# Kernel optimization log

Hardware: AMD Instinct MI355X
Metric: run time of the kernel (lower is better)

## Reference

```python
import jax, jax.numpy as jnp
import numpy as np

B, H, W, C = 128, 8, 32, 512
RNN = 512; EMB = 512; ATT = 512
VOCAB = 110          # vocab_size -> classes = VOCAB + 1
MAXLEN = 30          # loop runs MAXLEN + 1 steps


def setup_inputs() -> dict:
    key = jax.random.key(0)
    ks = jax.random.split(key, 16)
    w = lambda i, shape: jax.random.normal(ks[i], shape, jnp.float32) * 0.02
    return {
        "features": jax.random.normal(ks[0], (B, H, W, C), jnp.float32),
        "holistic": jax.random.normal(ks[1], (B, RNN), jnp.float32),
        "gt": jax.random.randint(ks[2], (B, MAXLEN + 1), 0, VOCAB + 1),
        "embed_W": w(3, (VOCAB + 1, EMB)),
        "k0": w(4, (EMB, 4 * RNN)), "rk0": w(5, (RNN, 4 * RNN)), "b0": jnp.zeros((4 * RNN,), jnp.float32),
        "k1": w(6, (RNN, 4 * RNN)), "rk1": w(7, (RNN, 4 * RNN)), "b1": jnp.zeros((4 * RNN,), jnp.float32),
        "Wh": w(8, (RNN, ATT)),                       # 1x1 conv on (B,1,1,RNN) == dense
        "Wf": w(9, (3, 3, C, ATT)), "bf": jnp.zeros((ATT,), jnp.float32),
        "wa": w(10, (ATT, 1)),                        # 1x1 conv -> scalar attention logit
        "out_W": w(11, (2 * RNN, VOCAB + 1)), "out_b": jnp.zeros((VOCAB + 1,), jnp.float32),
    }


def _lstm(x, h, c, k, rk, b):
    # Keras LSTMCell: gates order i, f, g(cell), o
    z = x @ k + h @ rk + b
    i, f, g, o = jnp.split(z, 4, axis=-1)
    c2 = jax.nn.sigmoid(f) * c + jax.nn.sigmoid(i) * jnp.tanh(g)
    h2 = jax.nn.sigmoid(o) * jnp.tanh(c2)
    return h2, c2


def reference(features, holistic, gt, embed_W, k0, rk0, b0, k1, rk1, b1,
              Wh, Wf, bf, wa, out_W, out_b):
    Bb, Hh, Ww, Cc = features.shape
    # features_projector (3x3 conv, SAME) is timestep-invariant: precompute once
    fproj = jax.lax.conv_general_dilated(
        features, Wf, (1, 1), "SAME",
        dimension_numbers=("NHWC", "HWIO", "NHWC")) + bf          # (B,H,W,ATT)

    zeros = jnp.zeros((Bb, RNN), features.dtype)
    # prime stacked LSTM with holistic vector (zero initial state)
    h0, c0 = _lstm(holistic, zeros, zeros, k0, rk0, b0)
    h1, c1 = _lstm(h0, zeros, zeros, k1, rk1, b1)

    # teacher forcing: step 0 uses SOS token = vocab_size+1 (out-of-range -> zero one-hot),
    # step t>0 uses gt[:, t-1]
    sos = jnp.full((1, Bb), VOCAB + 1, gt.dtype)
    symbols = jnp.concatenate([sos, gt[:, :MAXLEN].T], axis=0)     # (T, B), T = MAXLEN+1

    def step(carry, sym):
        h0, c0, h1, c1 = carry
        x = jax.nn.one_hot(sym, VOCAB + 1, dtype=features.dtype) @ embed_W   # (B, EMB)
        h0, c0 = _lstm(x, h0, c0, k0, rk0, b0)
        h1, c1 = _lstm(h0, h1, c1, k1, rk1, b1)
        # attention over conv feature map
        hp = h1 @ Wh                                               # (B, ATT)
        proj = jnp.tanh(fproj + hp[:, None, None, :])              # (B,H,W,ATT)
        att = (proj @ wa).reshape(Bb, Hh * Ww)                     # (B, H*W)
        att = jax.nn.softmax(att, axis=-1).reshape(Bb, Hh, Ww, 1)
        glimpse = jnp.sum(features * att, axis=(1, 2))             # (B, C)
        logits = jnp.concatenate([h1, glimpse], axis=-1) @ out_W + out_b
        return (h0, c0, h1, c1), logits

    _, logits = jax.lax.scan(step, (h0, c0, h1, c1), symbols)      # (T, B, VOCAB+1)
    return jnp.transpose(logits, (1, 0, 2))                        # (B, T, VOCAB+1)
```

## Files before the change

kernel.cpp:

```cpp
#include <hip/hip_runtime.h>


typedef __bf16 bf16;
typedef bf16 bf16x8 __attribute__((ext_vector_type(8)));
typedef float f32x4 __attribute__((ext_vector_type(4)));

#define MFMA16(a, b, c) __builtin_amdgcn_mfma_f32_16x16x32_bf16((a), (b), (c), 0, 0, 0)

__device__ __forceinline__ float b2f(unsigned short u) {
    return __uint_as_float(((unsigned int)u) << 16);
}
__device__ __forceinline__ unsigned short f2b(float f) {
    unsigned int x = __float_as_uint(f);
    unsigned int r = (x + 0x7fffu + ((x >> 16) & 1u)) >> 16;
    return (unsigned short)r;
}
__device__ __forceinline__ float exp2_raw(float x) {
    float r;
    asm("v_exp_f32 %0, %1" : "=v"(r) : "v"(x));
    return r;
}
__device__ __forceinline__ float tanh_fast(float x) {
    const float e = exp2_raw(2.885390082f * x);
    return 1.0f - 2.0f * __builtin_amdgcn_rcpf(e + 1.0f);
}
__device__ __forceinline__ float sig_fast(float x) {
    return __builtin_amdgcn_rcpf(1.0f + exp2_raw(-1.44269504f * x));
}
__device__ __forceinline__ void gl16(const ushort* g, ushort* l) {
    __builtin_amdgcn_global_load_lds(
        (const __attribute__((address_space(1))) void*)g,
        (__attribute__((address_space(3))) void*)l, 16, 0, 0);
}

__global__ void detect_dtype(const void* __restrict__ feat, int* __restrict__ flag) {
    if (threadIdx.x == 0 && blockIdx.x == 0) {
        const ushort* u = (const ushort*)feat;
        int cnt = 0;
        for (int i = 0; i < 128; i += 2) {
            const int e = (u[i] >> 7) & 0xFF;
            if (e >= 96 && e <= 150) ++cnt;
        }
        *flag = (cnt >= 40) ? 0 : 1;
    }
}

__global__ __launch_bounds__(256) void cvt_bf16(
    const void* __restrict__ src, ushort* __restrict__ dst, int n,
    const int* __restrict__ flag) {
    const int i = blockIdx.x * 256 + threadIdx.x;
    if (i >= n) return;
    if (*flag) dst[i] = f2b(((const float*)src)[i]);
    else       dst[i] = ((const ushort*)src)[i];
}

__global__ __launch_bounds__(256) void cvt_f32(
    const void* __restrict__ src, float* __restrict__ dst, int n,
    const int* __restrict__ flag) {
    const int i = blockIdx.x * 256 + threadIdx.x;
    if (i >= n) return;
    if (*flag) dst[i] = ((const float*)src)[i];
    else       dst[i] = b2f(((const ushort*)src)[i]);
}

__global__ __launch_bounds__(256) void build_featpad(
    const void* __restrict__ feat, ushort* __restrict__ featPad,
    const int* __restrict__ flag) {
    const int i = blockIdx.x * 256 + threadIdx.x;
    if (i >= 128 * 10 * 34 * 512) return;
    const int c = i & 511;
    const int xy = i >> 9;
    const int x = xy % 34;
    const int t2 = xy / 34;
    const int y = t2 % 10;
    const int b = t2 / 10;
    ushort v = 0;
    if (y >= 1 && y <= 8 && x >= 1 && x <= 32) {
        const size_t si = ((size_t)((b * 8 + y - 1) * 32 + (x - 1)) << 9) + c;
        v = *flag ? f2b(((const float*)feat)[si]) : ((const ushort*)feat)[si];
    }
    featPad[i] = v;
}

__global__ __launch_bounds__(256) void transpose_any(
    const void* __restrict__ in, ushort* __restrict__ out, int R, int C,
    const int* __restrict__ flag) {
    __shared__ float s[32][33];
    const int f32 = *flag;
    const int nbc = C >> 5;
    const int rb = blockIdx.x / nbc, cb = blockIdx.x % nbc;
    const int tx = threadIdx.x & 31, ty = threadIdx.x >> 5;
#pragma unroll
    for (int k = 0; k < 4; ++k) {
        const size_t idx = (size_t)(rb * 32 + ty + k * 8) * C + cb * 32 + tx;
        s[ty + k * 8][tx] = f32 ? ((const float*)in)[idx] : b2f(((const ushort*)in)[idx]);
    }
    __syncthreads();
#pragma unroll
    for (int k = 0; k < 4; ++k)
        out[(size_t)(cb * 32 + ty + k * 8) * R + rb * 32 + tx] = f2b(s[tx][ty + k * 8]);
}

__global__ __launch_bounds__(256) void woT_build(
    const float* __restrict__ outWf, ushort* __restrict__ WoTpad) {
    const int i = blockIdx.x * 256 + threadIdx.x;
    if (i >= 131072) return;
    const int v = i >> 10, k = i & 1023;
    WoTpad[i] = (v < 111) ? f2b(outWf[k * 111 + v]) : (ushort)0;
}

__global__ __launch_bounds__(256) void conv_fproj(
    const ushort* __restrict__ featPad, const ushort* __restrict__ WfT,
    const float* __restrict__ bff, ushort* __restrict__ fproj) {
    __shared__ __align__(16) ushort As[128 * 64];
    __shared__ __align__(16) ushort Bs[128 * 64];
    const int tid = threadIdx.x;
    const int nb = blockIdx.x >> 8;
    const int rb = blockIdx.x & 255;
    const int b = rb >> 1, p0 = (rb & 1) << 7;
    const int w = tid >> 6, lane = tid & 63, l15 = lane & 15, q = lane >> 4;
    const int wr = (w >> 1) << 6, wc = (w & 1) << 6;
    const int chunkoff = (((lane & 7) ^ (lane >> 3)) << 3);
    int aoff[4], boff[4];
#pragma unroll
    for (int i = 0; i < 4; ++i) {
        const int r = w * 32 + (lane >> 3) + i * 8;
        const int p = p0 + r;
        const int yy = p >> 5, xx = p & 31;
        aoff[i] = (((b * 10 + yy) * 34 + xx) << 9) + chunkoff;
        boff[i] = (nb * 128 + r) * 4608 + chunkoff;
    }
    const int swa = l15 & 7;
    f32x4 acc[4][4] = {};
    for (int kb = 0; kb < 72; ++kb) {
        const int tap = kb >> 3;
        const int dy = tap / 3, dx = tap - dy * 3;
        const int koffA = ((dy * 34 + dx) << 9) + ((kb & 7) << 6);
        const int koffB = kb * 64;
        __syncthreads();
#pragma unroll
        for (int i = 0; i < 4; ++i) {
            gl16(featPad + aoff[i] + koffA, &As[(w * 32 + i * 8) * 64]);
            gl16(WfT + boff[i] + koffB, &Bs[(w * 32 + i * 8) * 64]);
        }
        __syncthreads();
#pragma unroll
        for (int ks = 0; ks < 64; ks += 32) {
            const int cq = (ks >> 3) + q;
            const int col = ((cq ^ swa) << 3);
            bf16x8 af[4], bfr[4];
#pragma unroll
            for (int i = 0; i < 4; ++i) af[i] = *(const bf16x8*)&As[(wr + i * 16 + l15) * 64 + col];
#pragma unroll
            for (int j = 0; j < 4; ++j) bfr[j] = *(const bf16x8*)&Bs[(wc + j * 16 + l15) * 64 + col];
#pragma unroll
            for (int i = 0; i < 4; ++i)
#pragma unroll
                for (int j = 0; j < 4; ++j)
                    acc[i][j] = MFMA16(af[i], bfr[j], acc[i][j]);
        }
    }
    const int rowbase = rb * 128 + wr, colbase = nb * 128 + wc;
#pragma unroll
    for (int i = 0; i < 4; ++i)
#pragma unroll
        for (int j = 0; j < 4; ++j)
#pragma unroll
            for (int rr = 0; rr < 4; ++rr) {
                const int row = rowbase + i * 16 + q * 4 + rr;
                const int col = colbase + j * 16 + l15;
                fproj[(size_t)row * 512 + col] = f2b(acc[i][j][rr] + bff[col]);
            }
}

__global__ __launch_bounds__(256) void gemm_bt(
    const ushort* __restrict__ A, const ushort* __restrict__ BT,
    float* __restrict__ C, int M, int N, int K, int lda) {
    __shared__ __align__(16) bf16 As[128][72];
    __shared__ __align__(16) bf16 Bs[128][72];
    const int tid = threadIdx.x;
    const int nnb = N >> 7;
    const int rb = blockIdx.x / nnb, nb = blockIdx.x % nnb;
    const int ar = tid >> 1, ah = (tid & 1) << 5;
    const int w = tid >> 6, lane = tid & 63, l15 = lane & 15, q = lane >> 4;
    const int wr = (w >> 1) << 6, wc = (w & 1) << 6;
    const int r_glob = rb * 128 + ar;
    const bool aval = (r_glob < M);
    const int r_ld = aval ? r_glob : 0;
    f32x4 acc[4][4] = {};
    const int nkb = K >> 6;
    for (int kb = 0; kb < nkb; ++kb) {
        const uint4 z4 = {0u, 0u, 0u, 0u};
        const uint4* asrc = (const uint4*)(A + (size_t)r_ld * lda + kb * 64 + ah);
        uint4 a0 = asrc[0], a1 = asrc[1], a2 = asrc[2], a3 = asrc[3];
        if (!aval) { a0 = z4; a1 = z4; a2 = z4; a3 = z4; }
        const uint4* bsrc = (const uint4*)(BT + (size_t)(nb * 128 + ar) * K + kb * 64 + ah);
        uint4 b0v = bsrc[0], b1v = bsrc[1], b2v = bsrc[2], b3v = bsrc[3];
        __syncthreads();
        *(uint4*)&As[ar][ah] = a0;
        *(uint4*)&As[ar][ah + 8] = a1;
        *(uint4*)&As[ar][ah + 16] = a2;
        *(uint4*)&As[ar][ah + 24] = a3;
        *(uint4*)&Bs[ar][ah] = b0v;
        *(uint4*)&Bs[ar][ah + 8] = b1v;
        *(uint4*)&Bs[ar][ah + 16] = b2v;
        *(uint4*)&Bs[ar][ah + 24] = b3v;
        __syncthreads();
#pragma unroll
        for (int ks = 0; ks < 64; ks += 32) {
            bf16x8 af[4], bfr[4];
#pragma unroll
            for (int i = 0; i < 4; ++i) af[i] = *(const bf16x8*)&As[wr + i * 16 + l15][ks + q * 8];
#pragma unroll
            for (int j = 0; j < 4; ++j) bfr[j] = *(const bf16x8*)&Bs[wc + j * 16 + l15][ks + q * 8];
#pragma unroll
            for (int i = 0; i < 4; ++i)
#pragma unroll
                for (int j = 0; j < 4; ++j)
                    acc[i][j] = MFMA16(af[i], bfr[j], acc[i][j]);
        }
    }
#pragma unroll
    for (int i = 0; i < 4; ++i)
#pragma unroll
        for (int j = 0; j < 4; ++j)
#pragma unroll
            for (int rr = 0; rr < 4; ++rr) {
                const int row = rb * 128 + wr + i * 16 + q * 4 + rr;
                const int col = nb * 128 + wc + j * 16 + l15;
                if (row < M) C[(size_t)row * N + col] = acc[i][j][rr];
            }
}

__global__ __launch_bounds__(256) void lstm_stage(
    int t,
    const ushort* __restrict__ holistic, const int* __restrict__ gt,
    const float* __restrict__ b0f, const float* __restrict__ b1f,
    const ushort* __restrict__ k0T, const ushort* __restrict__ rk0T,
    const ushort* __restrict__ k1T, const ushort* __restrict__ rk1T,
    const float* __restrict__ E0,
    ushort* h0b0, ushort* h0b1, ushort* h1b0, ushort* h1b1,
    float* c0buf, float* c1buf, ushort* HG) {
    const int part = blockIdx.x >> 7;
    const int bi = blockIdx.x & 127;
    const ushort *A1 = nullptr, *A2 = nullptr, *B1 = nullptr, *B2 = nullptr;
    const float* bias = nullptr;
    ushort *hout = nullptr, *hout2 = nullptr;
    float* cbuf = nullptr;
    bool useC = false, useE = false;
    if (part == 0) {
        if (!(t == -2 || (t >= 0 && t <= 30))) return;
        bias = b0f; cbuf = c0buf;
        if (t == -2) { A1 = holistic; B1 = k0T; hout = h0b1; }
        else {
            A1 = ((t + 1) & 1) ? h0b1 : h0b0;
            B1 = rk0T;
            hout = (t & 1) ? h0b1 : h0b0;
            useC = true; useE = true;
        }
    } else {
        if (!(t == -1 || (t >= 1 && t <= 31))) return;
        bias = b1f; cbuf = c1buf;
        if (t == -1) { A1 = h0b1; B1 = k1T; hout = h1b1; }
        else {
            const int s = t - 1;
            A1 = (s & 1) ? h0b1 : h0b0;
            A2 = ((s + 1) & 1) ? h1b1 : h1b0;
            B1 = k1T; B2 = rk1T;
            hout = (s & 1) ? h1b1 : h1b0;
            hout2 = HG + (size_t)s * 131072;
            useC = true;
        }
    }
    const int m0 = (bi >> 5) << 5;
    const int cc0 = (bi & 31) << 4;
    const int tid = threadIdx.x;
    const int w = tid >> 6, lane = tid & 63, l15 = lane & 15, q = lane >> 4;
    __shared__ __align__(16) ushort As1[32 * 520];
    __shared__ __align__(16) ushort As2[32 * 520];
    __shared__ float zs[4][32][17];
#pragma unroll
    for (int it = 0; it < 8; ++it) {
        const int idx = tid + it * 256;
        const int row = idx >> 6, chv = idx & 63;
        *(uint4*)&As1[row * 520 + chv * 8] =
            *(const uint4*)(A1 + (size_t)(m0 + row) * 512 + chv * 8);
    }
    if (A2) {
#pragma unroll
        for (int it = 0; it < 8; ++it) {
            const int idx = tid + it * 256;
            const int row = idx >> 6, chv = idx & 63;
            *(uint4*)&As2[row * 520 + chv * 8] =
                *(const uint4*)(A2 + (size_t)(m0 + row) * 512 + chv * 8);
        }
    }
    __syncthreads();
    const int nkb = A2 ? 16 : 8;
    const size_t brow = (size_t)(w * 512 + cc0 + l15) * 512 + q * 8;
    auto bp = [&](int kb) -> const ushort* {
        const ushort* base = (kb < 8) ? B1 : B2;
        return base + brow + (kb & 7) * 64;
    };
    bf16x8 b0a = *(const bf16x8*)bp(0), b1a = *(const bf16x8*)(bp(0) + 32);
    bf16x8 b0b = *(const bf16x8*)bp(1), b1b = *(const bf16x8*)(bp(1) + 32);
    bf16x8 b0c = *(const bf16x8*)bp(2), b1c = *(const bf16x8*)(bp(2) + 32);
    f32x4 acc0 = {}, acc1 = {};
    for (int kb = 0; kb < nkb; ++kb) {
        const bf16x8 p0 = b0a, p1 = b1a;
        b0a = b0b; b1a = b1b; b0b = b0c; b1b = b1c;
        if (kb + 3 < nkb) {
            b0c = *(const bf16x8*)bp(kb + 3);
            b1c = *(const bf16x8*)(bp(kb + 3) + 32);
        }
        const ushort* asrc = (kb < 8) ? As1 : As2;
        const int kk = (kb & 7) * 64 + q * 8;
        bf16x8 a00 = *(const bf16x8*)&asrc[l15 * 520 + kk];
        bf16x8 a10 = *(const bf16x8*)&asrc[(16 + l15) * 520 + kk];
        bf16x8 a01 = *(const bf16x8*)&asrc[l15 * 520 + kk + 32];
        bf16x8 a11 = *(const bf16x8*)&asrc[(16 + l15) * 520 + kk + 32];
        acc0 = MFMA16(a00, p0, acc0);
        acc1 = MFMA16(a10, p0, acc1);
        acc0 = MFMA16(a01, p1, acc0);
        acc1 = MFMA16(a11, p1, acc1);
    }
#pragma unroll
    for (int rr = 0; rr < 4; ++rr) {
        zs[w][q * 4 + rr][l15] = acc0[rr];
        zs[w][16 + q * 4 + rr][l15] = acc1[rr];
    }
    __syncthreads();
#pragma unroll
    for (int it = 0; it < 2; ++it) {
        const int e = tid + it * 256;
        const int mm = e >> 4, cc = e & 15;
        const int brow2 = m0 + mm, col = cc0 + cc;
        float zi = zs[0][mm][cc] + bias[col];
        float zf = zs[1][mm][cc] + bias[512 + col];
        float zg = zs[2][mm][cc] + bias[1024 + col];
        float zo = zs[3][mm][cc] + bias[1536 + col];
        if (useE) {
            const int s = (t == 0) ? 111 : gt[brow2 * 31 + t - 1];
            if (s >= 0 && s < 111) {
                const float* er = E0 + (size_t)s * 2048;
                zi += er[col]; zf += er[512 + col]; zg += er[1024 + col]; zo += er[1536 + col];
            }
        }
        const float cp = useC ? cbuf[brow2 * 512 + col] : 0.0f;
        const float c2 = sig_fast(zf) * cp + sig_fast(zi) * tanh_fast(zg);
        const float h = sig_fast(zo) * tanh_fast(c2);
        cbuf[brow2 * 512 + col] = c2;
        hout[brow2 * 512 + col] = f2b(h);
        if (hout2) hout2[brow2 * 1024 + col] = f2b(h);
    }
}

__global__ __launch_bounds__(256) void att_logits(
    const ushort* __restrict__ fproj, const float* __restrict__ HP,
    const float* __restrict__ waf, float* __restrict__ attL) {
    __shared__ float hpS[16][512];
    __shared__ float waS[512];
    __shared__ float accS[128][17];
    const int tid = threadIdx.x;
    const int b = blockIdx.x >> 2, ph = (blockIdx.x >> 1) & 1, th = blockIdx.x & 1;
    const int t0 = th << 4, tc = th ? 15 : 16;
    const int pl = tid & 127, ch = tid >> 7;
    const int p = ph * 128 + pl;
    for (int i = tid; i < 16 * 512; i += 256) {
        const int tt = i >> 9, c = i & 511;
        hpS[tt][c] = (tt < tc) ? 2.885390082f * HP[((size_t)(t0 + tt) * 128 + b) * 512 + c] : 0.0f;
    }
    waS[tid] = -2.0f * waf[tid];
    if (tid < 256) waS[256 + tid] = -2.0f * waf[256 + tid];
    __syncthreads();
    float sumW = 0.f;
    {
        const float* wh = &waS[ch * 256];
        for (int c4 = 0; c4 < 64; ++c4) {
            const float4 wv = *(const float4*)&wh[c4 * 4];
            sumW += wv.x + wv.y + wv.z + wv.w;
        }
        sumW *= -0.5f;
    }
    float acc[16];
#pragma unroll
    for (int tt = 0; tt < 16; ++tt) acc[tt] = 0.f;
    const ushort* frow = fproj + (size_t)(b * 256 + p) * 512 + ch * 256;
    for (int c8 = 0; c8 < 32; ++c8) {
        const int cc = ch * 256 + c8 * 8;
        const uint4 fv = *(const uint4*)(frow + c8 * 8);
        float f[8];
        f[0] = b2f((unsigned short)(fv.x & 0xffff)); f[1] = b2f((unsigned short)(fv.x >> 16));
        f[2] = b2f((unsigned short)(fv.y & 0xffff)); f[3] = b2f((unsigned short)(fv.y >> 16));
        f[4] = b2f((unsigned short)(fv.z & 0xffff)); f[5] = b2f((unsigned short)(fv.z >> 16));
        f[6] = b2f((unsigned short)(fv.w & 0xffff)); f[7] = b2f((unsigned short)(fv.w >> 16));
#pragma unroll
        for (int j = 0; j < 8; ++j) f[j] *= 2.885390082f;
        const float4 w0 = *(const float4*)&waS[cc];
        const float4 w1 = *(const float4*)&waS[cc + 4];
#pragma unroll
        for (int tt = 0; tt < 16; ++tt) {
            const float4 h0 = *(const float4*)&hpS[tt][cc];
            const float4 h1 = *(const float4*)&hpS[tt][cc + 4];
            float s = acc[tt];
            s = fmaf(__builtin_amdgcn_rcpf(exp2_raw(f[0] + h0.x) + 1.0f), w0.x, s);
            s = fmaf(__builtin_amdgcn_rcpf(exp2_raw(f[1] + h0.y) + 1.0f), w0.y, s);
            s = fmaf(__builtin_amdgcn_rcpf(exp2_raw(f[2] + h0.z) + 1.0f), w0.z, s);
            s = fmaf(__builtin_amdgcn_rcpf(exp2_raw(f[3] + h0.w) + 1.0f), w0.w, s);
            s = fmaf(__builtin_amdgcn_rcpf(exp2_raw(f[4] + h1.x) + 1.0f), w1.x, s);
            s = fmaf(__builtin_amdgcn_rcpf(exp2_raw(f[5] + h1.y) + 1.0f), w1.y, s);
            s = fmaf(__builtin_amdgcn_rcpf(exp2_raw(f[6] + h1.z) + 1.0f), w1.z, s);
            s = fmaf(__builtin_amdgcn_rcpf(exp2_raw(f[7] + h1.w) + 1.0f), w1.w, s);
            acc[tt] = s;
        }
    }
    if (ch == 1) {
#pragma unroll
        for (int tt = 0; tt < 16; ++tt) accS[pl][tt] = acc[tt] + sumW;
    }
    __syncthreads();
    if (ch == 0) {
        for (int tt = 0; tt < tc; ++tt)
            attL[((size_t)(t0 + tt) * 128 + b) * 256 + p] = acc[tt] + sumW + accS[pl][tt];
    }
}

__global__ __launch_bounds__(256) void glimpse_kernel(
    const ushort* __restrict__ featPad, const float* __restrict__ attL,
    ushort* __restrict__ HG) {
    __shared__ __align__(16) float attT[256 * 36];
    const int tid = threadIdx.x;
    const int b = blockIdx.x >> 1, chh = blockIdx.x & 1;
    const int c0 = chh << 8;
    const int w = tid >> 6, lane = tid & 63;
    for (int i = tid; i < 31 * 256; i += 256) {
        const int tt = i >> 8, p = i & 255;
        attT[p * 36 + tt] = attL[((size_t)tt * 128 + b) * 256 + p];
    }
    __syncthreads();
    for (int tt = w; tt < 31; tt += 4) {
        float v0 = attT[lane * 36 + tt], v1 = attT[(lane + 64) * 36 + tt];
        float v2 = attT[(lane + 128) * 36 + tt], v3 = attT[(lane + 192) * 36 + tt];
        float mx = fmaxf(fmaxf(v0, v1), fmaxf(v2, v3));
#pragma unroll
        for (int m = 1; m < 64; m <<= 1) mx = fmaxf(mx, __shfl_xor(mx, m));
        const float e0 = exp2_raw((v0 - mx) * 1.44269504f);
        const float e1 = exp2_raw((v1 - mx) * 1.44269504f);
        const float e2 = exp2_raw((v2 - mx) * 1.44269504f);
        const float e3 = exp2_raw((v3 - mx) * 1.44269504f);
        float s = e0 + e1 + e2 + e3;
#pragma unroll
        for (int m = 1; m < 64; m <<= 1) s += __shfl_xor(s, m);
        const float r = 1.0f / s;
        attT[lane * 36 + tt] = e0 * r;  attT[(lane + 64) * 36 + tt] = e1 * r;
        attT[(lane + 128) * 36 + tt] = e2 * r;  attT[(lane + 192) * 36 + tt] = e3 * r;
    }
    __syncthreads();
    float acc[31];
#pragma unroll
    for (int tt = 0; tt < 31; ++tt) acc[tt] = 0.f;
    for (int p = 0; p < 256; ++p) {
        const size_t fi = (((size_t)(b * 10 + (p >> 5) + 1) * 34 + (p & 31) + 1) << 9) + c0 + tid;
        const float fv = b2f(featPad[fi]);
        const float4 a0 = *(const float4*)&attT[p * 36];
        const float4 a1 = *(const float4*)&attT[p * 36 + 4];
        const float4 a2 = *(const float4*)&attT[p * 36 + 8];
        const float4 a3 = *(const float4*)&attT[p * 36 + 12];
        const float4 a4 = *(const float4*)&attT[p * 36 + 16];
        const float4 a5 = *(const float4*)&attT[p * 36 + 20];
        const float4 a6 = *(const float4*)&attT[p * 36 + 24];
        const float4 a7 = *(const float4*)&attT[p * 36 + 28];
        acc[0] = fmaf(fv, a0.x, acc[0]);   acc[1] = fmaf(fv, a0.y, acc[1]);
        acc[2] = fmaf(fv, a0.z, acc[2]);   acc[3] = fmaf(fv, a0.w, acc[3]);
        acc[4] = fmaf(fv, a1.x, acc[4]);   acc[5] = fmaf(fv, a1.y, acc[5]);
        acc[6] = fmaf(fv, a1.z, acc[6]);   acc[7] = fmaf(fv, a1.w, acc[7]);
        acc[8] = fmaf(fv, a2.x, acc[8]);   acc[9] = fmaf(fv, a2.y, acc[9]);
        acc[10] = fmaf(fv, a2.z, acc[10]); acc[11] = fmaf(fv, a2.w, acc[11]);
        acc[12] = fmaf(fv, a3.x, acc[12]); acc[13] = fmaf(fv, a3.y, acc[13]);
        acc[14] = fmaf(fv, a3.z, acc[14]); acc[15] = fmaf(fv, a3.w, acc[15]);
        acc[16] = fmaf(fv, a4.x, acc[16]); acc[17] = fmaf(fv, a4.y, acc[17]);
        acc[18] = fmaf(fv, a4.z, acc[18]); acc[19] = fmaf(fv, a4.w, acc[19]);
        acc[20] = fmaf(fv, a5.x, acc[20]); acc[21] = fmaf(fv, a5.y, acc[21]);
        acc[22] = fmaf(fv, a5.z, acc[22]); acc[23] = fmaf(fv, a5.w, acc[23]);
        acc[24] = fmaf(fv, a6.x, acc[24]); acc[25] = fmaf(fv, a6.y, acc[25]);
        acc[26] = fmaf(fv, a6.z, acc[26]); acc[27] = fmaf(fv, a6.w, acc[27]);
        acc[28] = fmaf(fv, a7.x, acc[28]); acc[29] = fmaf(fv, a7.y, acc[29]);
        acc[30] = fmaf(fv, a7.z, acc[30]);
    }
#pragma unroll
    for (int tt = 0; tt < 31; ++tt)
        HG[((size_t)tt * 128 + b) * 1024 + 512 + c0 + tid] = f2b(acc[tt]);
}

__global__ __launch_bounds__(256) void logits_store(
    const float* __restrict__ C, const float* __restrict__ outBf,
    void* __restrict__ out, const int* __restrict__ flag) {
    const int i = blockIdx.x * 256 + threadIdx.x;
    if (i >= 3968 * 111) return;
    const int r = i / 111, v = i - r * 111;
    const int tt = r >> 7, b = r & 127;
    const float a = C[(size_t)r * 128 + v] + outBf[v];
    const size_t oi = ((size_t)b * 31 + tt) * 111 + v;
    if (*flag) ((float*)out)[oi] = a;
    else       ((ushort*)out)[oi] = f2b(a);
}

extern "C" void kernel_launch(void* const* d_in, const int* in_sizes, int n_in,
                              void* d_out, int out_size, void* d_ws, size_t ws_size,
                              hipStream_t stream) {
    (void)in_sizes; (void)n_in; (void)out_size;
    const void* features = d_in[0];
    const void* holistic = d_in[1];
    const int*  gt       = (const int*)d_in[2];
    const void* embed_W  = d_in[3];
    const void* k0 = d_in[4];
    const void* rk0 = d_in[5];
    const void* b0 = d_in[6];
    const void* k1 = d_in[7];
    const void* rk1 = d_in[8];
    const void* b1 = d_in[9];
    const void* Wh = d_in[10];
    const void* Wf = d_in[11];
    const void* bfv = d_in[12];
    const void* wa = d_in[13];
    const void* outW = d_in[14];
    const void* outB = d_in[15];

    char* ws = (char*)d_ws;
    size_t off = 0;
    auto take = [&](size_t bytes) -> char* {
        char* p = ws + off;
        off += (bytes + 255) & ~(size_t)255;
        return p;
    };
    int*    flag    = (int*)take(256);
    ushort* featPad = (ushort*)take(128ull * 10 * 34 * 512 * 2);
    ushort* holB  = (ushort*)take(65536ull * 2);
    ushort* embB  = (ushort*)take(56832ull * 2);
    float*  b0f   = (float*)take(2048ull * 4);
    float*  b1f   = (float*)take(2048ull * 4);
    float*  bff   = (float*)take(512ull * 4);
    float*  waf   = (float*)take(512ull * 4);
    float*  outBf = (float*)take(111ull * 4);
    float*  outWf = (float*)take(113664ull * 4);
    ushort* fproj = (ushort*)take(32768ull * 512 * 2);
    ushort* WfT   = (ushort*)take(4608ull * 512 * 2);
    ushort* k0T   = (ushort*)take(2048ull * 512 * 2);
    ushort* rk0T  = (ushort*)take(2048ull * 512 * 2);
    ushort* k1T   = (ushort*)take(2048ull * 512 * 2);
    ushort* rk1T  = (ushort*)take(2048ull * 512 * 2);
    ushort* WhT   = (ushort*)take(512ull * 512 * 2);
    float*  E0    = (float*)take(111ull * 2048 * 4);
    ushort* h0b0  = (ushort*)take(128ull * 512 * 2);
    ushort* h0b1  = (ushort*)take(128ull * 512 * 2);
    ushort* h1b0  = (ushort*)take(128ull * 512 * 2);
    ushort* h1b1  = (ushort*)take(128ull * 512 * 2);
    float*  c0buf = (float*)take(128ull * 512 * 4);
    float*  c1buf = (float*)take(128ull * 512 * 4);
    ushort* HG    = (ushort*)take(3968ull * 1024 * 2);
    float*  HP    = (float*)take(3968ull * 512 * 4);
    float*  attL  = (float*)take(31ull * 128 * 256 * 4);
    float*  Cout   = (float*)attL;
    ushort* WoTpad = (ushort*)((char*)attL + 3968ull * 128 * 4);
    if (off > ws_size) return;

    detect_dtype<<<dim3(1), dim3(64), 0, stream>>>(features, flag);
    build_featpad<<<dim3(87040), dim3(256), 0, stream>>>(features, featPad, flag);
    cvt_bf16<<<dim3(256), dim3(256), 0, stream>>>(holistic, holB, 65536, flag);
    cvt_bf16<<<dim3(222), dim3(256), 0, stream>>>(embed_W, embB, 56832, flag);
    cvt_f32<<<dim3(8), dim3(256), 0, stream>>>(b0, b0f, 2048, flag);
    cvt_f32<<<dim3(8), dim3(256), 0, stream>>>(b1, b1f, 2048, flag);
    cvt_f32<<<dim3(2), dim3(256), 0, stream>>>(bfv, bff, 512, flag);
    cvt_f32<<<dim3(2), dim3(256), 0, stream>>>(wa, waf, 512, flag);
    cvt_f32<<<dim3(1), dim3(256), 0, stream>>>(outB, outBf, 111, flag);
    cvt_f32<<<dim3(444), dim3(256), 0, stream>>>(outW, outWf, 113664, flag);
    transpose_any<<<dim3(16 * 64), dim3(256), 0, stream>>>(k0, k0T, 512, 2048, flag);
    transpose_any<<<dim3(16 * 64), dim3(256), 0, stream>>>(rk0, rk0T, 512, 2048, flag);
    transpose_any<<<dim3(16 * 64), dim3(256), 0, stream>>>(k1, k1T, 512, 2048, flag);
    transpose_any<<<dim3(16 * 64), dim3(256), 0, stream>>>(rk1, rk1T, 512, 2048, flag);
    transpose_any<<<dim3(16 * 16), dim3(256), 0, stream>>>(Wh, WhT, 512, 512, flag);
    transpose_any<<<dim3(144 * 16), dim3(256), 0, stream>>>(Wf, WfT, 4608, 512, flag);
    conv_fproj<<<dim3(1024), dim3(256), 0, stream>>>(featPad, WfT, bff, fproj);
    gemm_bt<<<dim3(16), dim3(256), 0, stream>>>(embB, k0T, E0, 111, 2048, 512, 512);
    for (int t = -2; t <= 31; ++t)
        lstm_stage<<<dim3(256), dim3(256), 0, stream>>>(t, holB, gt, b0f, b1f,
            k0T, rk0T, k1T, rk1T, E0, h0b0, h0b1, h1b0, h1b1, c0buf, c1buf, HG);
    gemm_bt<<<dim3(31 * 4), dim3(256), 0, stream>>>(HG, WhT, HP, 3968, 512, 512, 1024);
    att_logits<<<dim3(512), dim3(256), 0, stream>>>(fproj, HP, waf, attL);
    glimpse_kernel<<<dim3(256), dim3(256), 0, stream>>>(featPad, attL, HG);
    woT_build<<<dim3(512), dim3(256), 0, stream>>>(outWf, WoTpad);
    gemm_bt<<<dim3(31), dim3(256), 0, stream>>>(HG, WoTpad, Cout, 3968, 128, 1024, 1024);
    logits_store<<<dim3(1721), dim3(256), 0, stream>>>(Cout, outBf, d_out, flag);
}
```

Baseline: 933.4 us.

## Merge setup conversion kernels, fold tanh scale into conv, split att_logits finer

Collapses the many small conversion and transpose launches into two combined kernels, and builds the padded output weight directly from the raw input, which removes the intermediate fp32 copy. The 2.885 tanh prescale is moved into the conv epilogue so att_logits no longer multiplies each loaded feature. att_logits now handles 8 timesteps per block instead of 16 and launches twice as many blocks, trading more fproj rereads for higher occupancy and less register pressure. WoTpad gets its own workspace buffer instead of aliasing attL.

```diff
diff --git a/kernel.cpp b/kernel.cpp
--- a/kernel.cpp
+++ b/kernel.cpp
@@ -31,6 +31,9 @@
     __builtin_amdgcn_global_load_lds(
         (const __attribute__((address_space(1))) void*)g,
         (__attribute__((address_space(3))) void*)l, 16, 0, 0);
+}
+__device__ __forceinline__ float ld_any(const void* p, size_t i, int f32) {
+    return f32 ? ((const float*)p)[i] : b2f(((const ushort*)p)[i]);
 }
 
 __global__ void detect_dtype(const void* __restrict__ feat, int* __restrict__ flag) {
@@ -45,22 +48,26 @@
     }
 }
 
-__global__ __launch_bounds__(256) void cvt_bf16(
-    const void* __restrict__ src, ushort* __restrict__ dst, int n,
-    const int* __restrict__ flag) {
+__global__ __launch_bounds__(256) void setup_misc(
+    const void* holistic, const void* embed_W, const void* b0, const void* b1,
+    const void* bfv, const void* wa, const void* outB,
+    ushort* holB, ushort* embB, float* b0f, float* b1f,
+    float* bff, float* waf, float* outBf, const int* __restrict__ flag) {
     const int i = blockIdx.x * 256 + threadIdx.x;
-    if (i >= n) return;
-    if (*flag) dst[i] = f2b(((const float*)src)[i]);
-    else       dst[i] = ((const ushort*)src)[i];
-}
-
-__global__ __launch_bounds__(256) void cvt_f32(
-    const void* __restrict__ src, float* __restrict__ dst, int n,
-    const int* __restrict__ flag) {
-    const int i = blockIdx.x * 256 + threadIdx.x;
-    if (i >= n) return;
-    if (*flag) dst[i] = ((const float*)src)[i];
-    else       dst[i] = b2f(((const ushort*)src)[i]);
+    const int f32 = *flag;
+    if (i < 65536) { holB[i] = f2b(ld_any(holistic, i, f32)); return; }
+    int j = i - 65536;
+    if (j < 56832) { embB[j] = f2b(ld_any(embed_W, j, f32)); return; }
+    j -= 56832;
+    if (j < 2048) { b0f[j] = ld_any(b0, j, f32); return; }
+    j -= 2048;
+    if (j < 2048) { b1f[j] = ld_any(b1, j, f32); return; }
+    j -= 2048;
+    if (j < 512) { bff[j] = ld_any(bfv, j, f32); return; }
+    j -= 512;
+    if (j < 512) { waf[j] = ld_any(wa, j, f32); return; }
+    j -= 512;
+    if (j < 111) { outBf[j] = ld_any(outB, j, f32); return; }
 }
 
 __global__ __launch_bounds__(256) void build_featpad(
@@ -82,13 +89,11 @@
     featPad[i] = v;
 }
 
-__global__ __launch_bounds__(256) void transpose_any(
-    const void* __restrict__ in, ushort* __restrict__ out, int R, int C,
-    const int* __restrict__ flag) {
+__device__ __forceinline__ void transpose_body(
+    const void* in, ushort* out, int R, int C, int bid, int f32) {
     __shared__ float s[32][33];
-    const int f32 = *flag;
     const int nbc = C >> 5;
-    const int rb = blockIdx.x / nbc, cb = blockIdx.x % nbc;
+    const int rb = bid / nbc, cb = bid % nbc;
     const int tx = threadIdx.x & 31, ty = threadIdx.x >> 5;
 #pragma unroll
     for (int k = 0; k < 4; ++k) {
@@ -101,12 +106,28 @@
         out[(size_t)(cb * 32 + ty + k * 8) * R + rb * 32 + tx] = f2b(s[tx][ty + k * 8]);
 }
 
-__global__ __launch_bounds__(256) void woT_build(
-    const float* __restrict__ outWf, ushort* __restrict__ WoTpad) {
+__global__ __launch_bounds__(256) void transpose_all(
+    const void* k0, const void* rk0, const void* k1, const void* rk1,
+    const void* Wh, const void* Wf,
+    ushort* k0T, ushort* rk0T, ushort* k1T, ushort* rk1T,
+    ushort* WhT, ushort* WfT, const int* __restrict__ flag) {
+    const int f32 = *flag;
+    const int bid = blockIdx.x;
+    if (bid < 1024)      transpose_body(k0, k0T, 512, 2048, bid, f32);
+    else if (bid < 2048) transpose_body(rk0, rk0T, 512, 2048, bid - 1024, f32);
+    else if (bid < 3072) transpose_body(k1, k1T, 512, 2048, bid - 2048, f32);
+    else if (bid < 4096) transpose_body(rk1, rk1T, 512, 2048, bid - 3072, f32);
+    else if (bid < 4352) transpose_body(Wh, WhT, 512, 512, bid - 4096, f32);
+    else                 transpose_body(Wf, WfT, 4608, 512, bid - 4352, f32);
+}
+
+__global__ __launch_bounds__(256) void woT_build_any(
+    const void* __restrict__ outW, ushort* __restrict__ WoTpad,
+    const int* __restrict__ flag) {
     const int i = blockIdx.x * 256 + threadIdx.x;
     if (i >= 131072) return;
     const int v = i >> 10, k = i & 1023;
-    WoTpad[i] = (v < 111) ? f2b(outWf[k * 111 + v]) : (ushort)0;
+    WoTpad[i] = (v < 111) ? f2b(ld_any(outW, (size_t)k * 111 + v, *flag)) : (ushort)0;
 }
 
 __global__ __launch_bounds__(256) void conv_fproj(
@@ -169,7 +190,8 @@
             for (int rr = 0; rr < 4; ++rr) {
                 const int row = rowbase + i * 16 + q * 4 + rr;
                 const int col = colbase + j * 16 + l15;
-                fproj[(size_t)row * 512 + col] = f2b(acc[i][j][rr] + bff[col]);
+                fproj[(size_t)row * 512 + col] =
+                    f2b(2.885390082f * (acc[i][j][rr] + bff[col]));
             }
 }
 
@@ -358,15 +380,15 @@
 __global__ __launch_bounds__(256) void att_logits(
     const ushort* __restrict__ fproj, const float* __restrict__ HP,
     const float* __restrict__ waf, float* __restrict__ attL) {
-    __shared__ float hpS[16][512];
+    __shared__ float hpS[8][512];
     __shared__ float waS[512];
-    __shared__ float accS[128][17];
+    __shared__ float accS[128][9];
     const int tid = threadIdx.x;
-    const int b = blockIdx.x >> 2, ph = (blockIdx.x >> 1) & 1, th = blockIdx.x & 1;
-    const int t0 = th << 4, tc = th ? 15 : 16;
+    const int b = blockIdx.x >> 3, ph = (blockIdx.x >> 2) & 1, th = blockIdx.x & 3;
+    const int t0 = th << 3, tc = (th == 3) ? 7 : 8;
     const int pl = tid & 127, ch = tid >> 7;
     const int p = ph * 128 + pl;
-    for (int i = tid; i < 16 * 512; i += 256) {
+    for (int i = tid; i < 8 * 512; i += 256) {
         const int tt = i >> 9, c = i & 511;
         hpS[tt][c] = (tt < tc) ? 2.885390082f * HP[((size_t)(t0 + tt) * 128 + b) * 512 + c] : 0.0f;
     }
@@ -382,9 +404,9 @@
         }
         sumW *= -0.5f;
     }
-    float acc[16];
-#pragma unroll
-    for (int tt = 0; tt < 16; ++tt) acc[tt] = 0.f;
+    float acc[8];
+#pragma unroll
+    for (int tt = 0; tt < 8; ++tt) acc[tt] = 0.f;
     const ushort* frow = fproj + (size_t)(b * 256 + p) * 512 + ch * 256;
     for (int c8 = 0; c8 < 32; ++c8) {
         const int cc = ch * 256 + c8 * 8;
@@ -394,12 +416,10 @@
         f[2] = b2f((unsigned short)(fv.y & 0xffff)); f[3] = b2f((unsigned short)(fv.y >> 16));
         f[4] = b2f((unsigned short)(fv.z & 0xffff)); f[5] = b2f((unsigned short)(fv.z >> 16));
         f[6] = b2f((unsigned short)(fv.w & 0xffff)); f[7] = b2f((unsigned short)(fv.w >> 16));
-#pragma unroll
-        for (int j = 0; j < 8; ++j) f[j] *= 2.885390082f;
         const float4 w0 = *(const float4*)&waS[cc];
         const float4 w1 = *(const float4*)&waS[cc + 4];
 #pragma unroll
-        for (int tt = 0; tt < 16; ++tt) {
+        for (int tt = 0; tt < 8; ++tt) {
             const float4 h0 = *(const float4*)&hpS[tt][cc];
             const float4 h1 = *(const float4*)&hpS[tt][cc + 4];
             float s = acc[tt];
@@ -416,7 +436,7 @@
     }
     if (ch == 1) {
 #pragma unroll
-        for (int tt = 0; tt < 16; ++tt) accS[pl][tt] = acc[tt] + sumW;
+        for (int tt = 0; tt < 8; ++tt) accS[pl][tt] = acc[tt] + sumW;
     }
     __syncthreads();
     if (ch == 0) {
@@ -542,7 +562,7 @@
     float*  bff   = (float*)take(512ull * 4);
     float*  waf   = (float*)take(512ull * 4);
     float*  outBf = (float*)take(111ull * 4);
-    float*  outWf = (float*)take(113664ull * 4);
+    ushort* WoTpad = (ushort*)take(131072ull * 2);
     ushort* fproj = (ushort*)take(32768ull * 512 * 2);
     ushort* WfT   = (ushort*)take(4608ull * 512 * 2);
     ushort* k0T   = (ushort*)take(2048ull * 512 * 2);
@@ -560,35 +580,25 @@
     ushort* HG    = (ushort*)take(3968ull * 1024 * 2);
     float*  HP    = (float*)take(3968ull * 512 * 4);
     float*  attL  = (float*)take(31ull * 128 * 256 * 4);
-    float*  Cout   = (float*)attL;
-    ushort* WoTpad = (ushort*)((char*)attL + 3968ull * 128 * 4);
+    float*  Cout  = (float*)attL;
     if (off > ws_size) return;
 
     detect_dtype<<<dim3(1), dim3(64), 0, stream>>>(features, flag);
     build_featpad<<<dim3(87040), dim3(256), 0, stream>>>(features, featPad, flag);
-    cvt_bf16<<<dim3(256), dim3(256), 0, stream>>>(holistic, holB, 65536, flag);
-    cvt_bf16<<<dim3(222), dim3(256), 0, stream>>>(embed_W, embB, 56832, flag);
-    cvt_f32<<<dim3(8), dim3(256), 0, stream>>>(b0, b0f, 2048, flag);
-    cvt_f32<<<dim3(8), dim3(256), 0, stream>>>(b1, b1f, 2048, flag);
-    cvt_f32<<<dim3(2), dim3(256), 0, stream>>>(bfv, bff, 512, flag);
-    cvt_f32<<<dim3(2), dim3(256), 0, stream>>>(wa, waf, 512, flag);
-    cvt_f32<<<dim3(1), dim3(256), 0, stream>>>(outB, outBf, 111, flag);
-    cvt_f32<<<dim3(444), dim3(256), 0, stream>>>(outW, outWf, 113664, flag);
-    transpose_any<<<dim3(16 * 64), dim3(256), 0, stream>>>(k0, k0T, 512, 2048, flag);
-    transpose_any<<<dim3(16 * 64), dim3(256), 0, stream>>>(rk0, rk0T, 512, 2048, flag);
-    transpose_any<<<dim3(16 * 64), dim3(256), 0, stream>>>(k1, k1T, 512, 2048, flag);
-    transpose_any<<<dim3(16 * 64), dim3(256), 0, stream>>>(rk1, rk1T, 512, 2048, flag);
-    transpose_any<<<dim3(16 * 16), dim3(256), 0, stream>>>(Wh, WhT, 512, 512, flag);
-    transpose_any<<<dim3(144 * 16), dim3(256), 0, stream>>>(Wf, WfT, 4608, 512, flag);
+    setup_misc<<<dim3(499), dim3(256), 0, stream>>>(
+        holistic, embed_W, b0, b1, bfv, wa, outB,
+        holB, embB, b0f, b1f, bff, waf, outBf, flag);
+    transpose_all<<<dim3(6656), dim3(256), 0, stream>>>(
+        k0, rk0, k1, rk1, Wh, Wf, k0T, rk0T, k1T, rk1T, WhT, WfT, flag);
+    woT_build_any<<<dim3(512), dim3(256), 0, stream>>>(outW, WoTpad, flag);
     conv_fproj<<<dim3(1024), dim3(256), 0, stream>>>(featPad, WfT, bff, fproj);
     gemm_bt<<<dim3(16), dim3(256), 0, stream>>>(embB, k0T, E0, 111, 2048, 512, 512);
     for (int t = -2; t <= 31; ++t)
         lstm_stage<<<dim3(256), dim3(256), 0, stream>>>(t, holB, gt, b0f, b1f,
             k0T, rk0T, k1T, rk1T, E0, h0b0, h0b1, h1b0, h1b1, c0buf, c1buf, HG);
     gemm_bt<<<dim3(31 * 4), dim3(256), 0, stream>>>(HG, WhT, HP, 3968, 512, 512, 1024);
-    att_logits<<<dim3(512), dim3(256), 0, stream>>>(fproj, HP, waf, attL);
+    att_logits<<<dim3(1024), dim3(256), 0, stream>>>(fproj, HP, waf, attL);
     glimpse_kernel<<<dim3(256), dim3(256), 0, stream>>>(featPad, attL, HG);
-    woT_build<<<dim3(512), dim3(256), 0, stream>>>(outWf, WoTpad);
     gemm_bt<<<dim3(31), dim3(256), 0, stream>>>(HG, WoTpad, Cout, 3968, 128, 1024, 1024);
     logits_store<<<dim3(1721), dim3(256), 0, stream>>>(Cout, outBf, d_out, flag);
 }
```

Measured after the change: 915.2 us. No clear change (-1.9%).
